# Kernel tuning notes

Hardware: AMD Instinct MI355X
Metric: run time of the kernel (lower is better)

Reference implementation:

```python
import jax, jax.numpy as jnp
import numpy as np
from functools import partial

CHANNEL_N = 16
FIRE_RATE = 0.5
SCALE_GROWTH = 1.0
SCALE_GROWTH_SYNTH = 1.0
ANGLE = 0.0


def _sobel_kernels(angle, channel_n):
    # dx = outer([1,2,1],[-1,0,1])/8 ; dy = dx.T ; rotated by angle (degrees)
    dx = np.outer([1.0, 2.0, 1.0], [-1.0, 0.0, 1.0]) / 8.0
    dy = dx.T
    c, s = np.cos(angle * np.pi / 180.0), np.sin(angle * np.pi / 180.0)
    w1 = (c * dx - s * dy).astype(np.float32)
    w2 = (s * dx + c * dy).astype(np.float32)
    # depthwise conv weights, OIHW with O=channel_n, I=1 (groups=channel_n)
    k1 = jnp.asarray(np.tile(w1[None, None], (channel_n, 1, 1, 1)))
    k2 = jnp.asarray(np.tile(w2[None, None], (channel_n, 1, 1, 1)))
    return k1, k2


def _depthwise(x_nchw, k):
    return jax.lax.conv_general_dilated(
        x_nchw, k, window_strides=(1, 1), padding=((1, 1), (1, 1)),
        dimension_numbers=('NCHW', 'OIHW', 'NCHW'),
        feature_group_count=x_nchw.shape[1])


def _alive(x_nchw):
    # 3x3 max-pool (stride 1, pad 1) on channel 1, threshold 0.1
    a = x_nchw[:, 1:2]
    m = jax.lax.reduce_window(a, -jnp.inf, jax.lax.max,
                              (1, 1, 3, 3), (1, 1, 1, 1),
                              ((0, 0), (0, 0), (1, 1), (1, 1)))
    return m > 0.1


def _update(x, w0, b0, w1, key):
    # x: [B,H,W,C]; torch does x.transpose(1,3) -> [B,C,W,H]
    xt = jnp.transpose(x, (0, 3, 2, 1))
    pre_life = _alive(xt)
    k1, k2 = _sobel_kernels(ANGLE, xt.shape[1])
    y = jnp.concatenate([xt, _depthwise(xt, k1), _depthwise(xt, k2)], axis=1)  # [B,3C,W,H]
    d = jnp.transpose(y, (0, 3, 2, 1))  # [B,H,W,3C]
    h = jax.nn.relu(jnp.einsum('bhwc,cd->bhwd', d, w0) + b0)
    dx = jnp.einsum('bhwd,dc->bhwc', h, w1)
    stoch = (jax.random.uniform(key, dx.shape[:3] + (1,)) > FIRE_RATE).astype(dx.dtype)
    dx = dx * stoch * (SCALE_GROWTH * SCALE_GROWTH_SYNTH)
    xt = xt + jnp.transpose(dx, (0, 3, 2, 1))
    post_life = _alive(xt)
    xt = xt * (pre_life & post_life).astype(xt.dtype)
    return jnp.transpose(xt, (0, 3, 2, 1))


def setup_inputs() -> dict:
    key = jax.random.key(0)
    k1, k2, k3, k4 = jax.random.split(key, 4)
    B, H, W, C, HID = 16, 256, 256, CHANNEL_N, 128
    x = jax.random.uniform(k1, (B, H, W, C), dtype=jnp.float32)
    w0 = jax.random.normal(k2, (3 * C, HID), dtype=jnp.float32) * 0.05
    b0 = jax.random.normal(k3, (HID,), dtype=jnp.float32) * 0.05
    w1 = jax.random.normal(k4, (HID, C), dtype=jnp.float32) * 0.05
    return {'x': x, 'w0': w0, 'b0': b0, 'w1': w1, 'steps': 1}


def reference(x, w0, b0, w1, steps):
    key = jax.random.key(42)
    for step in range(steps):
        x = _update(x, w0, b0, w1, jax.random.fold_in(key, step))
    return x
```

## Files before the change

kernel.cpp:

```cpp
#include <hip/hip_runtime.h>
#include <hip/hip_bf16.h>

#define BB 16
#define HH 256
#define WW 256
#define CC 16
#define HID 128
#define NPIX (BB*HH*WW)
#define NBLK (BB*HH)

#define PCL_STRIDE 36
#define PCL_WAVE   (64*PCL_STRIDE)

typedef __attribute__((ext_vector_type(8))) short s16x8;
typedef __attribute__((ext_vector_type(4))) float f32x4;

union V8 { uint4 u; uint2 h[2]; s16x8 s; };

struct Key2 { unsigned a, b; };

__host__ __device__ constexpr unsigned rotl32c(unsigned x, int d) {
    return (x << d) | (x >> (32 - d));
}

__host__ __device__ constexpr Key2 tf2x32(unsigned k0, unsigned k1, unsigned x0, unsigned x1) {
    const unsigned ks2 = k0 ^ k1 ^ 0x1BD11BDAu;
    const int R[5][4] = {{13,15,26,6},{17,29,16,24},{13,15,26,6},{17,29,16,24},{13,15,26,6}};
    const unsigned ka[5] = {k1, ks2, k0, k1, ks2};
    const unsigned kb[5] = {ks2, k0, k1, ks2, k0};
    x0 += k0; x1 += k1;
    for (int i = 0; i < 5; ++i) {
        for (int j = 0; j < 4; ++j) { x0 += x1; x1 = rotl32c(x1, R[i][j]); x1 ^= x0; }
        x0 += ka[i]; x1 += kb[i] + (unsigned)(i + 1);
    }
    return Key2{x0, x1};
}
constexpr Key2 FK = tf2x32(0u, 42u, 0u, 0u);

__device__ inline unsigned pk2(float a, float b) {
    union { __hip_bfloat162 h2; unsigned u; } cv;
    cv.h2 = __float22bfloat162_rn(make_float2(a, b));
    return cv.u;
}

__global__ __launch_bounds__(256)
void ca_prep(const float* __restrict__ w0, const float* __restrict__ w1,
             short* __restrict__ w0bf, short* __restrict__ w1bf)
{
    const int t = threadIdx.x;
    const int blk = blockIdx.x;
    if (blk < 4) {
        const int row = blk * 256 + t;
        const int l15 = row & 15, g = (row >> 4) & 3, ks = (row >> 6) & 1;
        const int nt = (row >> 7) & 1, p = row >> 8;
        const int n = p * 32 + nt * 16 + l15;
        float v[8];
        #pragma unroll
        for (int jj = 0; jj < 8; ++jj) {
            const int kg = ks * 32 + g * 8 + jj;
            v[jj] = (kg < 48) ? w0[kg * HID + n] : 0.0f;
        }
        uint4 pkv;
        pkv.x = pk2(v[0], v[1]); pkv.y = pk2(v[2], v[3]);
        pkv.z = pk2(v[4], v[5]); pkv.w = pk2(v[6], v[7]);
        *reinterpret_cast<uint4*>(&w0bf[row * 8]) = pkv;
    } else {
        const int l15 = t & 15, g = (t >> 4) & 3, p = t >> 6;
        float v[8];
        #pragma unroll
        for (int e = 0; e < 8; ++e) v[e] = w1[(p * 32 + g * 8 + e) * CC + l15];
        uint4 pkv;
        pkv.x = pk2(v[0], v[1]); pkv.y = pk2(v[2], v[3]);
        pkv.z = pk2(v[4], v[5]); pkv.w = pk2(v[6], v[7]);
        *reinterpret_cast<uint4*>(&w1bf[t * 8]) = pkv;
    }
}

__global__ __launch_bounds__(256, 4)
void ca_fused(const float* __restrict__ x, const short* __restrict__ w0bf,
              const float* __restrict__ b0, const short* __restrict__ w1bf,
              float* __restrict__ out, float* __restrict__ ch1new,
              unsigned char* __restrict__ prelife)
{
    __shared__ short percL[4 * PCL_WAVE];
    __shared__ float slotL[4][34];
    __shared__ float slotR[4][34];

    const int tid = threadIdx.x;
    const unsigned bid = blockIdx.x;
    const unsigned lb = (bid & 7u) * 512u + (bid >> 3);
    const int h = lb & 255, b = lb >> 8;
    const unsigned jbase = lb << 8;
    const unsigned j = jbase + tid;
    const int wave = tid >> 6, lane = tid & 63;
    const int l15 = lane & 15, g = lane >> 4;

    const float* pB = x + (((size_t)b * HH + h) * WW + tid) * CC;
    float4 A4[4], B4[4], C4[4];
    #pragma unroll
    for (int q = 0; q < 4; ++q) B4[q] = *reinterpret_cast<const float4*>(pB + q * 4);
    if (h > 0) {
        const float* pA = pB - (size_t)WW * CC;
        #pragma unroll
        for (int q = 0; q < 4; ++q) A4[q] = *reinterpret_cast<const float4*>(pA + q * 4);
    } else {
        #pragma unroll
        for (int q = 0; q < 4; ++q) A4[q] = make_float4(0.f, 0.f, 0.f, 0.f);
    }
    if (h < HH - 1) {
        const float* pC = pB + (size_t)WW * CC;
        #pragma unroll
        for (int q = 0; q < 4; ++q) C4[q] = *reinterpret_cast<const float4*>(pC + q * 4);
    } else {
        #pragma unroll
        for (int q = 0; q < 4; ++q) C4[q] = make_float4(0.f, 0.f, 0.f, 0.f);
    }

    float D[16], S[16];
    #pragma unroll
    for (int q = 0; q < 4; ++q) {
        const float4 a = A4[q], bb = B4[q], c = C4[q];
        D[q*4+0] = c.x - a.x; D[q*4+1] = c.y - a.y;
        D[q*4+2] = c.z - a.z; D[q*4+3] = c.w - a.w;
        S[q*4+0] = fmaf(2.f, bb.x, a.x + c.x);
        S[q*4+1] = fmaf(2.f, bb.y, a.y + c.y);
        S[q*4+2] = fmaf(2.f, bb.z, a.z + c.z);
        S[q*4+3] = fmaf(2.f, bb.w, a.w + c.w);
    }
    const float M = fmaxf(fmaxf(A4[0].y, B4[0].y), C4[0].y);

    if (lane == 0) {
        float* sp = slotR[wave];
        #pragma unroll
        for (int c = 0; c < 16; ++c) { sp[c] = D[c]; sp[16 + c] = S[c]; }
        sp[32] = M;
    }
    if (lane == 63) {
        float* sp = slotL[wave];
        #pragma unroll
        for (int c = 0; c < 16; ++c) { sp[c] = D[c]; sp[16 + c] = S[c]; }
        sp[32] = M;
    }
    __syncthreads();

    float conv[32];
    #pragma unroll
    for (int hf = 0; hf < 2; ++hf) {
        const int c0 = hf * 8;
        float Dl[8], Dr[8], Sl[8], Sr[8];
        #pragma unroll
        for (int c = 0; c < 8; ++c) {
            Dl[c] = __shfl_up(D[c0 + c], 1);  Dr[c] = __shfl_down(D[c0 + c], 1);
            Sl[c] = __shfl_up(S[c0 + c], 1);  Sr[c] = __shfl_down(S[c0 + c], 1);
        }
        if (lane == 0) {
            if (tid == 0) {
                #pragma unroll
                for (int c = 0; c < 8; ++c) { Dl[c] = 0.f; Sl[c] = 0.f; }
            } else {
                const float* sp = slotL[wave - 1];
                #pragma unroll
                for (int c = 0; c < 8; ++c) { Dl[c] = sp[c0 + c]; Sl[c] = sp[16 + c0 + c]; }
            }
        }
        if (lane == 63) {
            if (tid == 255) {
                #pragma unroll
                for (int c = 0; c < 8; ++c) { Dr[c] = 0.f; Sr[c] = 0.f; }
            } else {
                const float* sp = slotR[wave + 1];
                #pragma unroll
                for (int c = 0; c < 8; ++c) { Dr[c] = sp[c0 + c]; Sr[c] = sp[16 + c0 + c]; }
            }
        }
        #pragma unroll
        for (int c = 0; c < 8; ++c) {
            conv[c0 + c]      = 0.125f * (Dl[c] + Dr[c] + 2.f * D[c0 + c]);
            conv[16 + c0 + c] = 0.125f * (Sr[c] - Sl[c]);
        }
    }

    float Ml = __shfl_up(M, 1), Mr = __shfl_down(M, 1);
    if (lane == 0)  Ml = (tid == 0)   ? -3.0e38f : slotL[wave - 1][32];
    if (lane == 63) Mr = (tid == 255) ? -3.0e38f : slotR[wave + 1][32];
    const float maxc1 = fmaxf(fmaxf(Ml, M), Mr);

    {
        const int base = wave * PCL_WAVE + lane * PCL_STRIDE;
        #pragma unroll
        for (int c = 0; c < 8; ++c) {
            uint2 pkv;
            pkv.x = pk2(conv[c*4 + 0], conv[c*4 + 1]);
            pkv.y = pk2(conv[c*4 + 2], conv[c*4 + 3]);
            *reinterpret_cast<uint2*>(&percL[base + c * 4]) = pkv;
        }
    }

    const Key2 r = tf2x32(FK.a, FK.b, 0u, j);
    const unsigned bits = r.a ^ r.b;
    const float uu = __uint_as_float((bits >> 9) | 0x3f800000u) - 1.0f;
    const unsigned long long kmask = __ballot(uu > 0.5f);
    prelife[j] = (maxc1 > 0.1f) ? (unsigned char)1 : (unsigned char)0;

    const unsigned pixbase = jbase + wave * 64;
    s16x8 pB0[4], pB1[4];
    #pragma unroll
    for (int mt = 0; mt < 4; ++mt) {
        const int prow = wave * PCL_WAVE + (mt * 16 + l15) * PCL_STRIDE;
        V8 f0, f1;
        if (g < 2) {
            const float* xp = &x[(size_t)(pixbase + mt * 16 + l15) * CC + g * 8];
            const float4 va = *reinterpret_cast<const float4*>(xp);
            const float4 vb = *reinterpret_cast<const float4*>(xp + 4);
            f0.u.x = pk2(va.x, va.y); f0.u.y = pk2(va.z, va.w);
            f0.u.z = pk2(vb.x, vb.y); f0.u.w = pk2(vb.z, vb.w);
            f1.h[0] = *reinterpret_cast<const uint2*>(&percL[prow + 16 + g * 8]);
            f1.h[1] = *reinterpret_cast<const uint2*>(&percL[prow + 16 + g * 8 + 4]);
        } else {
            f0.h[0] = *reinterpret_cast<const uint2*>(&percL[prow + (g - 2) * 8]);
            f0.h[1] = *reinterpret_cast<const uint2*>(&percL[prow + (g - 2) * 8 + 4]);
            f1.u = make_uint4(0u, 0u, 0u, 0u);
        }
        pB0[mt] = f0.s;
        pB1[mt] = f1.s;
    }

    __builtin_amdgcn_sched_barrier(0);

    const s16x8* w0F = reinterpret_cast<const s16x8*>(w0bf);
    const s16x8* w1F = reinterpret_cast<const s16x8*>(w1bf);

    short* HPw = &percL[wave * PCL_WAVE];
    f32x4 acc2[4];
    #pragma unroll
    for (int mt2 = 0; mt2 < 4; ++mt2) acc2[mt2] = 0.0f;

    #pragma unroll
    for (int p = 0; p < 4; ++p) {
        s16x8 w0f0[2], w0f1[2];
        #pragma unroll
        for (int nt = 0; nt < 2; ++nt) {
            w0f0[nt] = w0F[((p * 2 + nt) * 2 + 0) * 64 + lane];
            w0f1[nt] = w0F[((p * 2 + nt) * 2 + 1) * 64 + lane];
        }
        #pragma unroll
        for (int mt = 0; mt < 4; ++mt) {
            #pragma unroll
            for (int nt = 0; nt < 2; ++nt) {
                const float4 bv = *reinterpret_cast<const float4*>(&b0[p*32 + nt*16 + g*4]);
                f32x4 acc = {bv.x, bv.y, bv.z, bv.w};
                acc = __builtin_amdgcn_mfma_f32_16x16x32_bf16(w0f0[nt], pB0[mt], acc, 0, 0, 0);
                acc = __builtin_amdgcn_mfma_f32_16x16x32_bf16(w0f1[nt], pB1[mt], acc, 0, 0, 0);
                uint2 hv;
                hv.x = pk2(fmaxf(acc[0], 0.f), fmaxf(acc[1], 0.f));
                hv.y = pk2(fmaxf(acc[2], 0.f), fmaxf(acc[3], 0.f));
                const int m = mt * 16 + l15;
                *reinterpret_cast<uint2*>(
                    &HPw[m * 32 + 4 * ((4*nt + g) ^ (l15 & 6))]) = hv;
            }
        }
        {
            const s16x8 wf = w1F[p * 64 + lane];
            #pragma unroll
            for (int mt2 = 0; mt2 < 4; ++mt2) {
                const int m = mt2 * 16 + l15;
                const s16x8 hp = *reinterpret_cast<const s16x8*>(
                    &HPw[m * 32 + 4 * ((2*g) ^ (l15 & 6))]);
                acc2[mt2] = __builtin_amdgcn_mfma_f32_16x16x32_bf16(wf, hp, acc2[mt2], 0, 0, 0);
            }
        }
    }

    #pragma unroll
    for (int mt2 = 0; mt2 < 4; ++mt2) {
        const int prel = mt2 * 16 + l15;
        const unsigned pj = pixbase + prel;
        const float kv = ((kmask >> prel) & 1ull) ? 1.0f : 0.0f;
        const float4 x4 = *reinterpret_cast<const float4*>(&x[(size_t)pj * CC + g * 4]);
        float4 v;
        v.x = x4.x + acc2[mt2][0] * kv;
        v.y = x4.y + acc2[mt2][1] * kv;
        v.z = x4.z + acc2[mt2][2] * kv;
        v.w = x4.w + acc2[mt2][3] * kv;
        *reinterpret_cast<float4*>(&out[(size_t)pj * CC + g * 4]) = v;
        if (g == 0) ch1new[pj] = v.y;
    }
}

__global__ __launch_bounds__(256)
void ca_step2(float* __restrict__ out, const float* __restrict__ ch1new,
              const unsigned char* __restrict__ prelife)
{
    const int tid = threadIdx.x;
    const int lane = tid & 63;
    const int rowi = tid >> 6;
    const unsigned bid = blockIdx.x;
    const int hq = bid & 63, b = bid >> 6;
    const int h = hq * 4 + rowi;
    const unsigned rowbase = ((unsigned)(b * HH + h)) * WW;
    const int w0 = lane * 4;

    float4 vc = *reinterpret_cast<const float4*>(&ch1new[rowbase + w0]);
    float m0 = vc.x, m1 = vc.y, m2 = vc.z, m3 = vc.w;
    if (h > 0) {
        float4 vu = *reinterpret_cast<const float4*>(&ch1new[rowbase - WW + w0]);
        m0 = fmaxf(m0, vu.x); m1 = fmaxf(m1, vu.y); m2 = fmaxf(m2, vu.z); m3 = fmaxf(m3, vu.w);
    }
    if (h < HH - 1) {
        float4 vd = *reinterpret_cast<const float4*>(&ch1new[rowbase + WW + w0]);
        m0 = fmaxf(m0, vd.x); m1 = fmaxf(m1, vd.y); m2 = fmaxf(m2, vd.z); m3 = fmaxf(m3, vd.w);
    }
    float left  = __shfl_up(m3, 1);   if (lane == 0)  left  = -3.0e38f;
    float right = __shfl_down(m0, 1); if (lane == 63) right = -3.0e38f;

    float mm[4];
    mm[0] = fmaxf(fmaxf(left, m0), m1);
    mm[1] = fmaxf(fmaxf(m0, m1), m2);
    mm[2] = fmaxf(fmaxf(m1, m2), m3);
    mm[3] = fmaxf(fmaxf(m2, m3), right);

    const uchar4 pl = *reinterpret_cast<const uchar4*>(&prelife[rowbase + w0]);
    const unsigned char pla[4] = {pl.x, pl.y, pl.z, pl.w};
    #pragma unroll
    for (int i = 0; i < 4; ++i) {
        const bool alive = (pla[i] != 0) && (mm[i] > 0.1f);
        if (!alive) {
            const float4 z = make_float4(0.f, 0.f, 0.f, 0.f);
            float4* o = reinterpret_cast<float4*>(out + (size_t)(rowbase + w0 + i) * CC);
            o[0] = z; o[1] = z; o[2] = z; o[3] = z;
        }
    }
}

extern "C" void kernel_launch(void* const* d_in, const int* in_sizes, int n_in,
                              void* d_out, int out_size, void* d_ws, size_t ws_size,
                              hipStream_t stream) {
    const float* x  = (const float*)d_in[0];
    const float* w0 = (const float*)d_in[1];
    const float* b0 = (const float*)d_in[2];
    const float* w1 = (const float*)d_in[3];
    float* out = (float*)d_out;

    float* ch1new = (float*)d_ws;
    unsigned char* prelife = (unsigned char*)d_ws + (size_t)NPIX * 4;
    short* w0bf = (short*)((char*)d_ws + 5242880);
    short* w1bf = (short*)((char*)d_ws + 5242880 + 16384);

    ca_prep<<<dim3(5), dim3(256), 0, stream>>>(w0, w1, w0bf, w1bf);
    ca_fused<<<dim3(NBLK), dim3(256), 0, stream>>>(x, w0bf, b0, w1bf, out, ch1new, prelife);
    ca_step2<<<dim3(NPIX / 1024), dim3(256), 0, stream>>>(out, ch1new, prelife);
}
```

Before: 70.34 us.

## Process two image rows per block to reuse vertical Sobel halo loads

New measurement: 69.44 us. About the same (-1.3%).

```diff
diff --git a/kernel.cpp b/kernel.cpp
--- a/kernel.cpp
+++ b/kernel.cpp
@@ -7,10 +7,10 @@
 #define CC 16
 #define HID 128
 #define NPIX (BB*HH*WW)
-#define NBLK (BB*HH)
+#define NBLK2 2048
 
 #define PCL_STRIDE 36
-#define PCL_WAVE   (64*PCL_STRIDE)
+#define PCL_WAVE2  (128*PCL_STRIDE)
 
 typedef __attribute__((ext_vector_type(8))) short s16x8;
 typedef __attribute__((ext_vector_type(4))) float f32x4;
@@ -42,6 +42,8 @@
     cv.h2 = __float22bfloat162_rn(make_float2(a, b));
     return cv.u;
 }
+__device__ inline float unpk_lo(unsigned u) { return __uint_as_float(u << 16); }
+__device__ inline float unpk_hi(unsigned u) { return __uint_as_float(u & 0xffff0000u); }
 
 __global__ __launch_bounds__(256)
 void ca_prep(const float* __restrict__ w0, const float* __restrict__ w1,
@@ -82,111 +84,104 @@
               float* __restrict__ out, float* __restrict__ ch1new,
               unsigned char* __restrict__ prelife)
 {
-    __shared__ short percL[4 * PCL_WAVE];
-    __shared__ float slotL[4][34];
-    __shared__ float slotR[4][34];
+    __shared__ short percL[4 * PCL_WAVE2];
+    __shared__ unsigned slotLp[4][2][16];
+    __shared__ unsigned slotRp[4][2][16];
+    __shared__ float    slotLm[4][2];
+    __shared__ float    slotRm[4][2];
 
     const int tid = threadIdx.x;
     const unsigned bid = blockIdx.x;
-    const unsigned lb = (bid & 7u) * 512u + (bid >> 3);
-    const int h = lb & 255, b = lb >> 8;
-    const unsigned jbase = lb << 8;
-    const unsigned j = jbase + tid;
+    const unsigned lb = (bid & 7u) * 256u + (bid >> 3);
+    const int hpair = lb & 127;
+    const unsigned jbase = lb * 512u;
     const int wave = tid >> 6, lane = tid & 63;
     const int l15 = lane & 15, g = lane >> 4;
 
-    const float* pB = x + (((size_t)b * HH + h) * WW + tid) * CC;
-    float4 A4[4], B4[4], C4[4];
-    #pragma unroll
-    for (int q = 0; q < 4; ++q) B4[q] = *reinterpret_cast<const float4*>(pB + q * 4);
-    if (h > 0) {
-        const float* pA = pB - (size_t)WW * CC;
-        #pragma unroll
-        for (int q = 0; q < 4; ++q) A4[q] = *reinterpret_cast<const float4*>(pA + q * 4);
+    const float* pR1 = x + ((size_t)jbase + tid) * CC;
+    float4 R0[4], R1[4], R2[4], R3[4];
+    #pragma unroll
+    for (int q = 0; q < 4; ++q) R1[q] = *reinterpret_cast<const float4*>(pR1 + q * 4);
+    #pragma unroll
+    for (int q = 0; q < 4; ++q) R2[q] = *reinterpret_cast<const float4*>(pR1 + WW * CC + q * 4);
+    if (hpair > 0) {
+        #pragma unroll
+        for (int q = 0; q < 4; ++q) R0[q] = *reinterpret_cast<const float4*>(pR1 - WW * CC + q * 4);
     } else {
         #pragma unroll
-        for (int q = 0; q < 4; ++q) A4[q] = make_float4(0.f, 0.f, 0.f, 0.f);
-    }
-    if (h < HH - 1) {
-        const float* pC = pB + (size_t)WW * CC;
-        #pragma unroll
-        for (int q = 0; q < 4; ++q) C4[q] = *reinterpret_cast<const float4*>(pC + q * 4);
+        for (int q = 0; q < 4; ++q) R0[q] = make_float4(0.f, 0.f, 0.f, 0.f);
+    }
+    if (hpair < 127) {
+        #pragma unroll
+        for (int q = 0; q < 4; ++q) R3[q] = *reinterpret_cast<const float4*>(pR1 + 2 * WW * CC + q * 4);
     } else {
         #pragma unroll
-        for (int q = 0; q < 4; ++q) C4[q] = make_float4(0.f, 0.f, 0.f, 0.f);
-    }
-
-    float D[16], S[16];
+        for (int q = 0; q < 4; ++q) R3[q] = make_float4(0.f, 0.f, 0.f, 0.f);
+    }
+
+    unsigned pkA[16], pkB[16];
     #pragma unroll
     for (int q = 0; q < 4; ++q) {
-        const float4 a = A4[q], bb = B4[q], c = C4[q];
-        D[q*4+0] = c.x - a.x; D[q*4+1] = c.y - a.y;
-        D[q*4+2] = c.z - a.z; D[q*4+3] = c.w - a.w;
-        S[q*4+0] = fmaf(2.f, bb.x, a.x + c.x);
-        S[q*4+1] = fmaf(2.f, bb.y, a.y + c.y);
-        S[q*4+2] = fmaf(2.f, bb.z, a.z + c.z);
-        S[q*4+3] = fmaf(2.f, bb.w, a.w + c.w);
-    }
-    const float M = fmaxf(fmaxf(A4[0].y, B4[0].y), C4[0].y);
+        const float4 a = R0[q], bb = R1[q], c = R2[q], d = R3[q];
+        const float a_[4] = {a.x, a.y, a.z, a.w};
+        const float b_[4] = {bb.x, bb.y, bb.z, bb.w};
+        const float c_[4] = {c.x, c.y, c.z, c.w};
+        const float d_[4] = {d.x, d.y, d.z, d.w};
+        #pragma unroll
+        for (int e = 0; e < 4; ++e) {
+            const int ch = q * 4 + e;
+            pkA[ch] = pk2(c_[e] - a_[e], fmaf(2.f, b_[e], a_[e] + c_[e]));
+            pkB[ch] = pk2(d_[e] - b_[e], fmaf(2.f, c_[e], b_[e] + d_[e]));
+        }
+    }
+    const float M1 = fmaxf(fmaxf(R0[0].y, R1[0].y), R2[0].y);
+    const float M2 = fmaxf(fmaxf(R1[0].y, R2[0].y), R3[0].y);
 
     if (lane == 0) {
-        float* sp = slotR[wave];
-        #pragma unroll
-        for (int c = 0; c < 16; ++c) { sp[c] = D[c]; sp[16 + c] = S[c]; }
-        sp[32] = M;
+        #pragma unroll
+        for (int c = 0; c < 16; ++c) { slotRp[wave][0][c] = pkA[c]; slotRp[wave][1][c] = pkB[c]; }
+        slotRm[wave][0] = M1; slotRm[wave][1] = M2;
     }
     if (lane == 63) {
-        float* sp = slotL[wave];
-        #pragma unroll
-        for (int c = 0; c < 16; ++c) { sp[c] = D[c]; sp[16 + c] = S[c]; }
-        sp[32] = M;
+        #pragma unroll
+        for (int c = 0; c < 16; ++c) { slotLp[wave][0][c] = pkA[c]; slotLp[wave][1][c] = pkB[c]; }
+        slotLm[wave][0] = M1; slotLm[wave][1] = M2;
     }
     __syncthreads();
 
-    float conv[32];
-    #pragma unroll
-    for (int hf = 0; hf < 2; ++hf) {
-        const int c0 = hf * 8;
-        float Dl[8], Dr[8], Sl[8], Sr[8];
-        #pragma unroll
-        for (int c = 0; c < 8; ++c) {
-            Dl[c] = __shfl_up(D[c0 + c], 1);  Dr[c] = __shfl_down(D[c0 + c], 1);
-            Sl[c] = __shfl_up(S[c0 + c], 1);  Sr[c] = __shfl_down(S[c0 + c], 1);
-        }
-        if (lane == 0) {
-            if (tid == 0) {
+    unsigned long long kmask[2];
+    float maxc1v[2];
+    #pragma unroll
+    for (int rs = 0; rs < 2; ++rs) {
+        const unsigned* pk = (rs == 0) ? pkA : pkB;
+        float conv[32];
+        #pragma unroll
+        for (int hf = 0; hf < 2; ++hf) {
+            const int c0 = hf * 8;
+            unsigned pL[8], pR[8];
+            #pragma unroll
+            for (int c = 0; c < 8; ++c) {
+                pL[c] = __shfl_up(pk[c0 + c], 1);
+                pR[c] = __shfl_down(pk[c0 + c], 1);
+            }
+            if (lane == 0) {
                 #pragma unroll
-                for (int c = 0; c < 8; ++c) { Dl[c] = 0.f; Sl[c] = 0.f; }
-            } else {
-                const float* sp = slotL[wave - 1];
+                for (int c = 0; c < 8; ++c)
+                    pL[c] = (tid == 0) ? 0u : slotLp[wave - 1][rs][c0 + c];
+            }
+            if (lane == 63) {
                 #pragma unroll
-                for (int c = 0; c < 8; ++c) { Dl[c] = sp[c0 + c]; Sl[c] = sp[16 + c0 + c]; }
-            }
-        }
-        if (lane == 63) {
-            if (tid == 255) {
-                #pragma unroll
-                for (int c = 0; c < 8; ++c) { Dr[c] = 0.f; Sr[c] = 0.f; }
-            } else {
-                const float* sp = slotR[wave + 1];
-                #pragma unroll
-                for (int c = 0; c < 8; ++c) { Dr[c] = sp[c0 + c]; Sr[c] = sp[16 + c0 + c]; }
-            }
-        }
-        #pragma unroll
-        for (int c = 0; c < 8; ++c) {
-            conv[c0 + c]      = 0.125f * (Dl[c] + Dr[c] + 2.f * D[c0 + c]);
-            conv[16 + c0 + c] = 0.125f * (Sr[c] - Sl[c]);
-        }
-    }
-
-    float Ml = __shfl_up(M, 1), Mr = __shfl_down(M, 1);
-    if (lane == 0)  Ml = (tid == 0)   ? -3.0e38f : slotL[wave - 1][32];
-    if (lane == 63) Mr = (tid == 255) ? -3.0e38f : slotR[wave + 1][32];
-    const float maxc1 = fmaxf(fmaxf(Ml, M), Mr);
-
-    {
-        const int base = wave * PCL_WAVE + lane * PCL_STRIDE;
+                for (int c = 0; c < 8; ++c)
+                    pR[c] = (tid == 255) ? 0u : slotRp[wave + 1][rs][c0 + c];
+            }
+            #pragma unroll
+            for (int c = 0; c < 8; ++c) {
+                const float Dm = unpk_lo(pk[c0 + c]);
+                conv[c0 + c]      = 0.125f * (unpk_lo(pL[c]) + unpk_lo(pR[c]) + 2.f * Dm);
+                conv[16 + c0 + c] = 0.125f * (unpk_hi(pR[c]) - unpk_hi(pL[c]));
+            }
+        }
+        const int base = wave * PCL_WAVE2 + (rs * 64 + lane) * PCL_STRIDE;
         #pragma unroll
         for (int c = 0; c < 8; ++c) {
             uint2 pkv;
@@ -194,96 +189,106 @@
             pkv.y = pk2(conv[c*4 + 2], conv[c*4 + 3]);
             *reinterpret_cast<uint2*>(&percL[base + c * 4]) = pkv;
         }
-    }
-
-    const Key2 r = tf2x32(FK.a, FK.b, 0u, j);
-    const unsigned bits = r.a ^ r.b;
-    const float uu = __uint_as_float((bits >> 9) | 0x3f800000u) - 1.0f;
-    const unsigned long long kmask = __ballot(uu > 0.5f);
-    prelife[j] = (maxc1 > 0.1f) ? (unsigned char)1 : (unsigned char)0;
-
-    const unsigned pixbase = jbase + wave * 64;
-    s16x8 pB0[4], pB1[4];
-    #pragma unroll
-    for (int mt = 0; mt < 4; ++mt) {
-        const int prow = wave * PCL_WAVE + (mt * 16 + l15) * PCL_STRIDE;
-        V8 f0, f1;
-        if (g < 2) {
-            const float* xp = &x[(size_t)(pixbase + mt * 16 + l15) * CC + g * 8];
-            const float4 va = *reinterpret_cast<const float4*>(xp);
-            const float4 vb = *reinterpret_cast<const float4*>(xp + 4);
-            f0.u.x = pk2(va.x, va.y); f0.u.y = pk2(va.z, va.w);
-            f0.u.z = pk2(vb.x, vb.y); f0.u.w = pk2(vb.z, vb.w);
-            f1.h[0] = *reinterpret_cast<const uint2*>(&percL[prow + 16 + g * 8]);
-            f1.h[1] = *reinterpret_cast<const uint2*>(&percL[prow + 16 + g * 8 + 4]);
-        } else {
-            f0.h[0] = *reinterpret_cast<const uint2*>(&percL[prow + (g - 2) * 8]);
-            f0.h[1] = *reinterpret_cast<const uint2*>(&percL[prow + (g - 2) * 8 + 4]);
-            f1.u = make_uint4(0u, 0u, 0u, 0u);
-        }
-        pB0[mt] = f0.s;
-        pB1[mt] = f1.s;
-    }
-
-    __builtin_amdgcn_sched_barrier(0);
+        const float M = (rs == 0) ? M1 : M2;
+        float Ml = __shfl_up(M, 1), Mr = __shfl_down(M, 1);
+        if (lane == 0)  Ml = (tid == 0)   ? -3.0e38f : slotLm[wave - 1][rs];
+        if (lane == 63) Mr = (tid == 255) ? -3.0e38f : slotRm[wave + 1][rs];
+        maxc1v[rs] = fmaxf(fmaxf(Ml, M), Mr);
+        const unsigned j = jbase + rs * 256 + tid;
+        const Key2 r = tf2x32(FK.a, FK.b, 0u, j);
+        const unsigned bits = r.a ^ r.b;
+        const float uu = __uint_as_float((bits >> 9) | 0x3f800000u) - 1.0f;
+        kmask[rs] = __ballot(uu > 0.5f);
+        prelife[j] = (maxc1v[rs] > 0.1f) ? (unsigned char)1 : (unsigned char)0;
+    }
 
     const s16x8* w0F = reinterpret_cast<const s16x8*>(w0bf);
     const s16x8* w1F = reinterpret_cast<const s16x8*>(w1bf);
 
-    short* HPw = &percL[wave * PCL_WAVE];
-    f32x4 acc2[4];
-    #pragma unroll
-    for (int mt2 = 0; mt2 < 4; ++mt2) acc2[mt2] = 0.0f;
-
-    #pragma unroll
-    for (int p = 0; p < 4; ++p) {
-        s16x8 w0f0[2], w0f1[2];
-        #pragma unroll
-        for (int nt = 0; nt < 2; ++nt) {
-            w0f0[nt] = w0F[((p * 2 + nt) * 2 + 0) * 64 + lane];
-            w0f1[nt] = w0F[((p * 2 + nt) * 2 + 1) * 64 + lane];
-        }
+    #pragma unroll
+    for (int rs = 0; rs < 2; ++rs) {
+        const unsigned pixbase = jbase + rs * 256 + wave * 64;
+        const int halfbase = wave * PCL_WAVE2 + rs * 64 * PCL_STRIDE;
+
+        s16x8 pB0[4], pB1[4];
         #pragma unroll
         for (int mt = 0; mt < 4; ++mt) {
+            const int prow = halfbase + (mt * 16 + l15) * PCL_STRIDE;
+            V8 f0, f1;
+            if (g < 2) {
+                const float* xp = &x[(size_t)(pixbase + mt * 16 + l15) * CC + g * 8];
+                const float4 va = *reinterpret_cast<const float4*>(xp);
+                const float4 vb = *reinterpret_cast<const float4*>(xp + 4);
+                f0.u.x = pk2(va.x, va.y); f0.u.y = pk2(va.z, va.w);
+                f0.u.z = pk2(vb.x, vb.y); f0.u.w = pk2(vb.z, vb.w);
+                f1.h[0] = *reinterpret_cast<const uint2*>(&percL[prow + 16 + g * 8]);
+                f1.h[1] = *reinterpret_cast<const uint2*>(&percL[prow + 16 + g * 8 + 4]);
+            } else {
+                f0.h[0] = *reinterpret_cast<const uint2*>(&percL[prow + (g - 2) * 8]);
+                f0.h[1] = *reinterpret_cast<const uint2*>(&percL[prow + (g - 2) * 8 + 4]);
+                f1.u = make_uint4(0u, 0u, 0u, 0u);
+            }
+            pB0[mt] = f0.s;
+            pB1[mt] = f1.s;
+        }
+
+        __builtin_amdgcn_sched_barrier(0);
+
+        short* HPw = &percL[halfbase];
+        f32x4 acc2[4];
+        #pragma unroll
+        for (int mt2 = 0; mt2 < 4; ++mt2) acc2[mt2] = 0.0f;
+
+        #pragma unroll
+        for (int p = 0; p < 4; ++p) {
+            s16x8 w0f0[2], w0f1[2];
             #pragma unroll
             for (int nt = 0; nt < 2; ++nt) {
-                const float4 bv = *reinterpret_cast<const float4*>(&b0[p*32 + nt*16 + g*4]);
-                f32x4 acc = {bv.x, bv.y, bv.z, bv.w};
-                acc = __builtin_amdgcn_mfma_f32_16x16x32_bf16(w0f0[nt], pB0[mt], acc, 0, 0, 0);
-                acc = __builtin_amdgcn_mfma_f32_16x16x32_bf16(w0f1[nt], pB1[mt], acc, 0, 0, 0);
-                uint2 hv;
-                hv.x = pk2(fmaxf(acc[0], 0.f), fmaxf(acc[1], 0.f));
-                hv.y = pk2(fmaxf(acc[2], 0.f), fmaxf(acc[3], 0.f));
-                const int m = mt * 16 + l15;
-                *reinterpret_cast<uint2*>(
-                    &HPw[m * 32 + 4 * ((4*nt + g) ^ (l15 & 6))]) = hv;
-            }
-        }
-        {
-            const s16x8 wf = w1F[p * 64 + lane];
+                w0f0[nt] = w0F[((p * 2 + nt) * 2 + 0) * 64 + lane];
+                w0f1[nt] = w0F[((p * 2 + nt) * 2 + 1) * 64 + lane];
+            }
             #pragma unroll
-            for (int mt2 = 0; mt2 < 4; ++mt2) {
-                const int m = mt2 * 16 + l15;
-                const s16x8 hp = *reinterpret_cast<const s16x8*>(
-                    &HPw[m * 32 + 4 * ((2*g) ^ (l15 & 6))]);
-                acc2[mt2] = __builtin_amdgcn_mfma_f32_16x16x32_bf16(wf, hp, acc2[mt2], 0, 0, 0);
-            }
-        }
-    }
-
-    #pragma unroll
-    for (int mt2 = 0; mt2 < 4; ++mt2) {
-        const int prel = mt2 * 16 + l15;
-        const unsigned pj = pixbase + prel;
-        const float kv = ((kmask >> prel) & 1ull) ? 1.0f : 0.0f;
-        const float4 x4 = *reinterpret_cast<const float4*>(&x[(size_t)pj * CC + g * 4]);
-        float4 v;
-        v.x = x4.x + acc2[mt2][0] * kv;
-        v.y = x4.y + acc2[mt2][1] * kv;
-        v.z = x4.z + acc2[mt2][2] * kv;
-        v.w = x4.w + acc2[mt2][3] * kv;
-        *reinterpret_cast<float4*>(&out[(size_t)pj * CC + g * 4]) = v;
-        if (g == 0) ch1new[pj] = v.y;
+            for (int mt = 0; mt < 4; ++mt) {
+                #pragma unroll
+                for (int nt = 0; nt < 2; ++nt) {
+                    const float4 bv = *reinterpret_cast<const float4*>(&b0[p*32 + nt*16 + g*4]);
+                    f32x4 acc = {bv.x, bv.y, bv.z, bv.w};
+                    acc = __builtin_amdgcn_mfma_f32_16x16x32_bf16(w0f0[nt], pB0[mt], acc, 0, 0, 0);
+                    acc = __builtin_amdgcn_mfma_f32_16x16x32_bf16(w0f1[nt], pB1[mt], acc, 0, 0, 0);
+                    uint2 hv;
+                    hv.x = pk2(fmaxf(acc[0], 0.f), fmaxf(acc[1], 0.f));
+                    hv.y = pk2(fmaxf(acc[2], 0.f), fmaxf(acc[3], 0.f));
+                    const int m = mt * 16 + l15;
+                    *reinterpret_cast<uint2*>(
+                        &HPw[m * 32 + 4 * ((4*nt + g) ^ (l15 & 6))]) = hv;
+                }
+            }
+            {
+                const s16x8 wf = w1F[p * 64 + lane];
+                #pragma unroll
+                for (int mt2 = 0; mt2 < 4; ++mt2) {
+                    const int m = mt2 * 16 + l15;
+                    const s16x8 hp = *reinterpret_cast<const s16x8*>(
+                        &HPw[m * 32 + 4 * ((2*g) ^ (l15 & 6))]);
+                    acc2[mt2] = __builtin_amdgcn_mfma_f32_16x16x32_bf16(wf, hp, acc2[mt2], 0, 0, 0);
+                }
+            }
+        }
+
+        #pragma unroll
+        for (int mt2 = 0; mt2 < 4; ++mt2) {
+            const int prel = mt2 * 16 + l15;
+            const unsigned pj = pixbase + prel;
+            const float kv = ((kmask[rs] >> prel) & 1ull) ? 1.0f : 0.0f;
+            const float4 x4 = *reinterpret_cast<const float4*>(&x[(size_t)pj * CC + g * 4]);
+            float4 v;
+            v.x = x4.x + acc2[mt2][0] * kv;
+            v.y = x4.y + acc2[mt2][1] * kv;
+            v.z = x4.z + acc2[mt2][2] * kv;
+            v.w = x4.w + acc2[mt2][3] * kv;
+            *reinterpret_cast<float4*>(&out[(size_t)pj * CC + g * 4]) = v;
+            if (g == 0) ch1new[pj] = v.y;
+        }
     }
 }
 
@@ -347,6 +352,6 @@
     short* w1bf = (short*)((char*)d_ws + 5242880 + 16384);
 
     ca_prep<<<dim3(5), dim3(256), 0, stream>>>(w0, w1, w0bf, w1bf);
-    ca_fused<<<dim3(NBLK), dim3(256), 0, stream>>>(x, w0bf, b0, w1bf, out, ch1new, prelife);
+    ca_fused<<<dim3(NBLK2), dim3(256), 0, stream>>>(x, w0bf, b0, w1bf, out, ch1new, prelife);
     ca_step2<<<dim3(NPIX / 1024), dim3(256), 0, stream>>>(out, ch1new, prelife);
 }
```
